# Performance work log

Hardware: AMD Instinct MI355X
Metric: run time of the kernel (lower is better)

## Reference

```python
import jax, jax.numpy as jnp
import numpy as np

N = 100_000      # nodes
E = 3_200_000    # edges (avg degree 32)
F = 16           # irrep feature channels
IR = 4           # (max_l+1)**2 with max_l = 1
DENOM = 32.0     # denominator init kwarg
EPS = 1e-9
INV_S3 = 1.0 / np.sqrt(3.0).astype(np.float32)  # CG norm for 1x1->0
INV_S2 = 1.0 / np.sqrt(2.0).astype(np.float32)  # CG norm for 1x1->1


def setup_inputs() -> dict:
    key = jax.random.key(0)
    k0, k1, k2, k3, k4 = jax.random.split(key, 5)
    positions = jax.random.normal(k0, (N, 3), jnp.float32)
    node_feats = jax.random.normal(k1, (N, F, IR), jnp.float32)
    W = jax.random.normal(k2, (IR, IR), jnp.float32) / np.float32(np.sqrt(IR))
    b = jnp.zeros((IR,), jnp.float32)
    senders = jax.random.randint(k3, (E,), 0, N)
    receivers = jax.random.randint(k4, (E,), 0, N)
    return dict(positions=positions, node_feats=node_feats, W=W, b=b,
                senders=senders, receivers=receivers)


def reference(positions, node_feats, W, b, senders, receivers):
    # --- edge update: SH of normalized relative position, CG tensor product ---
    d = positions[receivers] - positions[senders]               # [E, 3]
    d = d / (jnp.linalg.norm(d, axis=-1, keepdims=True) + EPS)  # unit direction
    # real spherical harmonics up to l=1: sh0 = 1, sh1 = unit direction
    sh1 = d[:, None, :]                                         # [E, 1, 3]

    x = node_feats[senders]                                     # [E, F, 4]
    x0 = x[..., 0:1]                                            # l=0 part [E,F,1]
    x1 = x[..., 1:4]                                            # l=1 part [E,F,3]

    # CG paths with l3 <= max_l = 1:
    #   0x0->0 (identity), 1x1->0 (dot / sqrt3)
    out0 = x0 + jnp.sum(x1 * sh1, axis=-1, keepdims=True) * INV_S3      # [E,F,1]
    #   0x1->1, 1x0->1 (identities), 1x1->1 (cross / sqrt2)
    cross = jnp.cross(x1, jnp.broadcast_to(sh1, x1.shape))
    out1 = x0 * sh1 + x1 + cross * INV_S2                               # [E,F,3]
    tp = jnp.concatenate([out0, out1], axis=-1)                         # [E,F,4]

    # --- node update: segment-sum over receivers, scale, Dense over coeff dim ---
    agg = jax.ops.segment_sum(tp, receivers, num_segments=positions.shape[0])
    agg = agg / DENOM                                                   # [N,F,4]
    return agg @ W + b                                                  # [N,F,4]
```

## Files before the change

### kernel.cpp

```cpp
#include <hip/hip_runtime.h>


#define F_DIM 16
#define BIN_SHIFT 6
#define BIN_NODES (1 << BIN_SHIFT)
#define HALF_NODES (BIN_NODES / 2)
#define CHUNK 8192
#define CAP_LDS 1408
#define MAXBINS 2048

__global__ void __launch_bounds__(256) init_kernel(int* __restrict__ binCur,
                                                   int nbins, int cap)
{
    int b = blockIdx.x * blockDim.x + threadIdx.x;
    if (b < nbins) binCur[b] = b * cap;
}

__global__ void __launch_bounds__(256) pos_pack_kernel(
    const float* __restrict__ pos, float4* __restrict__ posf4, int N)
{
    int n = blockIdx.x * blockDim.x + threadIdx.x;
    if (n >= N) return;
    posf4[n] = make_float4(pos[3*n], pos[3*n+1], pos[3*n+2], 0.f);
}

__global__ void __launch_bounds__(512) build_bins_kernel(
    const int* __restrict__ senders, const int* __restrict__ receivers,
    int* __restrict__ binCur, int* __restrict__ bins,
    int nbins, int cap, int E)
{
    __shared__ int hbase[MAXBINS];
    __shared__ int hrank[MAXBINS];
    int t = threadIdx.x;
    for (int i = t; i < nbins; i += 512) { hbase[i] = 0; hrank[i] = 0; }
    __syncthreads();

    int base = blockIdx.x * CHUNK;
    int end  = base + CHUNK; if (end > E) end = E;

    for (int e = base + t; e < end; e += 512)
        atomicAdd(&hbase[((unsigned)receivers[e]) >> BIN_SHIFT], 1);
    __syncthreads();

    for (int i = t; i < nbins; i += 512) {
        int c = hbase[i];
        hbase[i] = (c > 0) ? atomicAdd(&binCur[i], c) : 0;
    }
    __syncthreads();

    for (int e = base + t; e < end; e += 512) {
        int r = receivers[e];
        int s = senders[e];
        int bb = r >> BIN_SHIFT;
        int rank = atomicAdd(&hrank[bb], 1);
        int dest = hbase[bb] + rank;
        if (dest < (bb + 1) * cap)
            bins[dest] = (s << BIN_SHIFT) | (r & (BIN_NODES - 1));
    }
}

__device__ __forceinline__ void edge_acc_d(
    float dx, float dy, float dz, const float4& fx,
    float& a0, float& a1, float& a2, float& a3)
{
    const float INV_S3 = 0.5773502691896258f;
    const float INV_S2 = 0.7071067811865476f;
    float dot = fx.y*dx + fx.z*dy + fx.w*dz;
    a0 += fx.x + dot * INV_S3;
    float c0 = fx.z*dz - fx.w*dy;
    float c1 = fx.w*dx - fx.y*dz;
    float c2 = fx.y*dy - fx.z*dx;
    a1 += fx.x*dx + fx.y + c0 * INV_S2;
    a2 += fx.x*dy + fx.z + c1 * INV_S2;
    a3 += fx.x*dz + fx.w + c2 * INV_S2;
}

__global__ void __launch_bounds__(256) bin_gather_kernel(
    const float4* __restrict__ posf4,
    const float* __restrict__ nf,
    const int* __restrict__ bins,
    const int* __restrict__ binCur,
    const float* __restrict__ W,
    const float* __restrict__ Bias,
    float* __restrict__ out,
    int N, int cap)
{
    __shared__ float4 ledge[CAP_LDS];
    __shared__ int lhist[HALF_NODES];
    __shared__ int lscan[HALF_NODES];
    __shared__ int lstart[HALF_NODES];

    int t = threadIdx.x;
    int bin  = blockIdx.x >> 1;
    int half = blockIdx.x & 1;
    int node0 = (bin << BIN_SHIFT) + half * HALF_NODES;
    int gbase = bin * cap;

    int cnt = binCur[bin] - gbase;
    if (cnt > cap) cnt = cap;

    if (t < HALF_NODES) lhist[t] = 0;
    __syncthreads();

    for (int j = t; j < cnt; j += 256) {
        int rl = bins[gbase + j] & (BIN_NODES - 1);
        if ((rl >> 5) == half) atomicAdd(&lhist[rl & (HALF_NODES - 1)], 1);
    }
    __syncthreads();

    if (t < HALF_NODES) lscan[t] = lhist[t];
    __syncthreads();
    for (int off = 1; off < HALF_NODES; off <<= 1) {
        int v = (t < HALF_NODES && t >= off) ? lscan[t - off] : 0;
        __syncthreads();
        if (t < HALF_NODES) lscan[t] += v;
        __syncthreads();
    }
    if (t < HALF_NODES) { lstart[t] = lscan[t] - lhist[t]; lhist[t] = 0; }
    __syncthreads();

    for (int j = t; j < cnt; j += 256) {
        int pk = bins[gbase + j];
        int rl = pk & (BIN_NODES - 1);
        if ((rl >> 5) != half) continue;
        int rl32 = rl & (HALF_NODES - 1);
        int s = pk >> BIN_SHIFT;
        int rank = atomicAdd(&lhist[rl32], 1);
        int dest = lstart[rl32] + rank;
        if (dest >= CAP_LDS) continue;
        float4 ps = posf4[s];
        float4 pr = posf4[node0 + rl32];
        float dx = pr.x - ps.x;
        float dy = pr.y - ps.y;
        float dz = pr.z - ps.z;
        float d2 = dx*dx + dy*dy + dz*dz;
        float inv = __builtin_amdgcn_rsqf(fmaxf(d2, 1e-18f));
        float4 rec;
        rec.x = dx * inv;
        rec.y = dy * inv;
        rec.z = dz * inv;
        rec.w = __int_as_float(s);
        ledge[dest] = rec;
    }
    __syncthreads();

    float w[16];
#pragma unroll
    for (int i = 0; i < 16; ++i) w[i] = W[i];
    float b0 = Bias[0], b1 = Bias[1], b2 = Bias[2], b3 = Bias[3];
    const float sc = 1.0f / 32.0f;

    int f = t & 15;
    const float4* nf4 = (const float4*)nf;

    for (int nl = t >> 4; nl < HALF_NODES; nl += 16) {
        int n = node0 + nl;
        if (n >= N) break;
        int s0 = lstart[nl];
        int dcnt = lscan[nl] - s0;
        if (dcnt > CAP_LDS - s0) dcnt = CAP_LDS - s0;

        float a0 = 0.f, a1 = 0.f, a2 = 0.f, a3 = 0.f;
        int j = 0;
        for (; j + 4 <= dcnt; j += 4) {
            float4 e0 = ledge[s0 + j + 0];
            float4 e1 = ledge[s0 + j + 1];
            float4 e2 = ledge[s0 + j + 2];
            float4 e3 = ledge[s0 + j + 3];
            int s_0 = __float_as_int(e0.w);
            int s_1 = __float_as_int(e1.w);
            int s_2 = __float_as_int(e2.w);
            int s_3 = __float_as_int(e3.w);
            float4 q0 = nf4[(unsigned)(s_0 * F_DIM + f)];
            float4 q1 = nf4[(unsigned)(s_1 * F_DIM + f)];
            float4 q2 = nf4[(unsigned)(s_2 * F_DIM + f)];
            float4 q3 = nf4[(unsigned)(s_3 * F_DIM + f)];
            edge_acc_d(e0.x, e0.y, e0.z, q0, a0, a1, a2, a3);
            edge_acc_d(e1.x, e1.y, e1.z, q1, a0, a1, a2, a3);
            edge_acc_d(e2.x, e2.y, e2.z, q2, a0, a1, a2, a3);
            edge_acc_d(e3.x, e3.y, e3.z, q3, a0, a1, a2, a3);
        }
        for (; j < dcnt; ++j) {
            float4 e0 = ledge[s0 + j];
            int s = __float_as_int(e0.w);
            float4 q = nf4[(unsigned)(s * F_DIM + f)];
            edge_acc_d(e0.x, e0.y, e0.z, q, a0, a1, a2, a3);
        }

        a0 *= sc; a1 *= sc; a2 *= sc; a3 *= sc;
        float4 o;
        o.x = a0*w[0] + a1*w[4] + a2*w[8]  + a3*w[12] + b0;
        o.y = a0*w[1] + a1*w[5] + a2*w[9]  + a3*w[13] + b1;
        o.z = a0*w[2] + a1*w[6] + a2*w[10] + a3*w[14] + b2;
        o.w = a0*w[3] + a1*w[7] + a2*w[11] + a3*w[15] + b3;
        ((float4*)out)[(size_t)n * F_DIM + f] = o;
    }
}

__global__ void __launch_bounds__(256) hist_kernel(
    const int* __restrict__ receivers, int* __restrict__ deg,
    int* __restrict__ rank, int E)
{
    int e = blockIdx.x * blockDim.x + threadIdx.x;
    if (e >= E) return;
    rank[e] = atomicAdd(&deg[receivers[e]], 1);
}

__global__ void __launch_bounds__(256) alloc_kernel(
    const int* __restrict__ deg, int* __restrict__ start,
    int* __restrict__ cursor, int N)
{
    __shared__ int tmp[256];
    __shared__ int base;
    int t = threadIdx.x;
    int n = blockIdx.x * blockDim.x + t;
    int v = (n < N) ? deg[n] : 0;
    tmp[t] = v;
    __syncthreads();
    for (int off = 1; off < 256; off <<= 1) {
        int x = (t >= off) ? tmp[t - off] : 0;
        __syncthreads();
        tmp[t] += x;
        __syncthreads();
    }
    int incl = tmp[t];
    if (t == 255) base = atomicAdd(cursor, incl);
    __syncthreads();
    if (n < N) start[n] = base + incl - v;
}

__global__ void __launch_bounds__(256) scatter_kernel(
    const int* __restrict__ senders, const int* __restrict__ receivers,
    const int* __restrict__ rank, const int* __restrict__ start,
    int* __restrict__ csr_s, int E)
{
    int e = blockIdx.x * blockDim.x + threadIdx.x;
    if (e >= E) return;
    csr_s[start[receivers[e]] + rank[e]] = senders[e];
}

__global__ void __launch_bounds__(256) gather_kernel(
    const float* __restrict__ pos,
    const float* __restrict__ nf,
    const int* __restrict__ csr_s,
    const int* __restrict__ start,
    const int* __restrict__ deg,
    const float* __restrict__ W,
    const float* __restrict__ b,
    float* __restrict__ out,
    int N)
{
    const float INV_S3 = 0.5773502691896258f;
    const float INV_S2 = 0.7071067811865476f;

    int tid = blockIdx.x * blockDim.x + threadIdx.x;
    int n = tid >> 4;
    if (n >= N) return;
    int f = tid & 15;

    float rx = pos[3*n], ry = pos[3*n+1], rz = pos[3*n+2];
    int s0 = start[n];
    int dcnt = deg[n];
    float a0 = 0.f, a1 = 0.f, a2 = 0.f, a3 = 0.f;
    const float4* nf4 = (const float4*)nf;

    int s = (dcnt > 0) ? csr_s[s0] : 0;
    for (int j = 0; j < dcnt; ++j) {
        int s_next = (j + 1 < dcnt) ? csr_s[s0 + j + 1] : 0;
        float dx = rx - pos[3*s], dy = ry - pos[3*s+1], dz = rz - pos[3*s+2];
        float d2 = dx*dx + dy*dy + dz*dz;
        float inv = __builtin_amdgcn_rsqf(fmaxf(d2, 1e-18f));
        dx *= inv; dy *= inv; dz *= inv;
        float4 x = nf4[(unsigned)(s * F_DIM + f)];
        float x0 = x.x, x1 = x.y, x2 = x.z, x3 = x.w;
        float dot = x1*dx + x2*dy + x3*dz;
        a0 += x0 + dot * INV_S3;
        float c0 = x2*dz - x3*dy, c1 = x3*dx - x1*dz, c2 = x1*dy - x2*dx;
        a1 += x0*dx + x1 + c0 * INV_S2;
        a2 += x0*dy + x2 + c1 * INV_S2;
        a3 += x0*dz + x3 + c2 * INV_S2;
        s = s_next;
    }
    const float sc = 1.0f / 32.0f;
    a0 *= sc; a1 *= sc; a2 *= sc; a3 *= sc;
    float4 o;
    o.x = a0*W[0] + a1*W[4] + a2*W[8]  + a3*W[12] + b[0];
    o.y = a0*W[1] + a1*W[5] + a2*W[9]  + a3*W[13] + b[1];
    o.z = a0*W[2] + a1*W[6] + a2*W[10] + a3*W[14] + b[2];
    o.w = a0*W[3] + a1*W[7] + a2*W[11] + a3*W[15] + b[3];
    ((float4*)out)[tid] = o;
}

extern "C" void kernel_launch(void* const* d_in, const int* in_sizes, int n_in,
                              void* d_out, int out_size, void* d_ws, size_t ws_size,
                              hipStream_t stream)
{
    const float* pos       = (const float*)d_in[0];
    const float* nf        = (const float*)d_in[1];
    const float* W         = (const float*)d_in[2];
    const float* b         = (const float*)d_in[3];
    const int*   senders   = (const int*)d_in[4];
    const int*   receivers = (const int*)d_in[5];

    int N = in_sizes[0] / 3;
    int E = in_sizes[4];
    float* out = (float*)d_out;
    const int blk = 256;

    int nbins = (N + BIN_NODES - 1) >> BIN_SHIFT;
    int cap   = E / nbins + 453;
    size_t need = ((size_t)N * 4 + (size_t)nbins * cap + nbins) * sizeof(float);

    if (nbins <= MAXBINS && ws_size >= need) {
        float4* posf4 = (float4*)d_ws;
        int* binCur = (int*)(posf4 + N);
        int* bins   = binCur + nbins;

        pos_pack_kernel<<<(N + blk - 1) / blk, blk, 0, stream>>>(pos, posf4, N);
        init_kernel<<<(nbins + blk - 1) / blk, blk, 0, stream>>>(binCur, nbins, cap);
        build_bins_kernel<<<(E + CHUNK - 1) / CHUNK, 512, 0, stream>>>(
            senders, receivers, binCur, bins, nbins, cap, E);
        bin_gather_kernel<<<nbins * 2, blk, 0, stream>>>(
            posf4, nf, bins, binCur, W, b, out, N, cap);
    } else {
        int* cursor = (int*)d_ws;
        int* deg    = cursor + 1;
        int* start  = deg + N;
        int* rank   = start + N;
        int* csr_s  = rank + E;

        hipMemsetAsync(cursor, 0, (size_t)(1 + N) * sizeof(int), stream);
        hist_kernel<<<(E + blk - 1) / blk, blk, 0, stream>>>(receivers, deg, rank, E);
        alloc_kernel<<<(N + blk - 1) / blk, blk, 0, stream>>>(deg, start, cursor, N);
        scatter_kernel<<<(E + blk - 1) / blk, blk, 0, stream>>>(
            senders, receivers, rank, start, csr_s, E);
        long total = (long)N * F_DIM;
        gather_kernel<<<(unsigned)((total + blk - 1) / blk), blk, 0, stream>>>(
            pos, nf, csr_s, start, deg, W, b, out, N);
    }
}
```

Measured before the change: 290.3 us.

## Gather node features as fp16 and fuse pack/init kernels

Adds a pack kernel that converts node features to half precision once per call, and merges it with the position packing and bin-cursor init into a single launch. The gather kernel then reads 8-byte half4 values per edge instead of 16-byte float4, halving random-gather traffic. The cost is an extra full pass over node features each call and reduced input precision, which may exceed tolerance. The fallback gather loop also drops its sender-index prefetch.

```diff
diff --git a/kernel.cpp b/kernel.cpp
--- a/kernel.cpp
+++ b/kernel.cpp
@@ -1,4 +1,5 @@
 #include <hip/hip_runtime.h>
+#include <hip/hip_fp16.h>
 
 
 #define F_DIM 16
@@ -9,19 +10,26 @@
 #define CAP_LDS 1408
 #define MAXBINS 2048
 
-__global__ void __launch_bounds__(256) init_kernel(int* __restrict__ binCur,
-                                                   int nbins, int cap)
-{
-    int b = blockIdx.x * blockDim.x + threadIdx.x;
-    if (b < nbins) binCur[b] = b * cap;
-}
-
-__global__ void __launch_bounds__(256) pos_pack_kernel(
-    const float* __restrict__ pos, float4* __restrict__ posf4, int N)
-{
-    int n = blockIdx.x * blockDim.x + threadIdx.x;
-    if (n >= N) return;
-    posf4[n] = make_float4(pos[3*n], pos[3*n+1], pos[3*n+2], 0.f);
+__global__ void __launch_bounds__(256) pack_kernel(
+    const float* __restrict__ pos, const float* __restrict__ nf,
+    float4* __restrict__ posf4, uint2* __restrict__ nfh,
+    int* __restrict__ binCur, int N, int nbins, int cap)
+{
+    int tid = blockIdx.x * blockDim.x + threadIdx.x;
+    int total = N * F_DIM;
+    if (tid < total) {
+        float4 q = ((const float4*)nf)[tid];
+        __half2 h01 = __floats2half2_rn(q.x, q.y);
+        __half2 h23 = __floats2half2_rn(q.z, q.w);
+        uint2 u;
+        u.x = *reinterpret_cast<unsigned*>(&h01);
+        u.y = *reinterpret_cast<unsigned*>(&h23);
+        nfh[tid] = u;
+    }
+    if (tid < N)
+        posf4[tid] = make_float4(pos[3*tid], pos[3*tid+1], pos[3*tid+2], 0.f);
+    if (tid < nbins)
+        binCur[tid] = tid * cap;
 }
 
 __global__ void __launch_bounds__(512) build_bins_kernel(
@@ -57,6 +65,15 @@
         if (dest < (bb + 1) * cap)
             bins[dest] = (s << BIN_SHIFT) | (r & (BIN_NODES - 1));
     }
+}
+
+__device__ __forceinline__ float4 unpack_h4(uint2 u)
+{
+    __half2 h01 = *reinterpret_cast<__half2*>(&u.x);
+    __half2 h23 = *reinterpret_cast<__half2*>(&u.y);
+    float2 a = __half22float2(h01);
+    float2 b = __half22float2(h23);
+    return make_float4(a.x, a.y, b.x, b.y);
 }
 
 __device__ __forceinline__ void edge_acc_d(
@@ -77,7 +94,7 @@
 
 __global__ void __launch_bounds__(256) bin_gather_kernel(
     const float4* __restrict__ posf4,
-    const float* __restrict__ nf,
+    const uint2* __restrict__ nfh,
     const int* __restrict__ bins,
     const int* __restrict__ binCur,
     const float* __restrict__ W,
@@ -151,7 +168,6 @@
     const float sc = 1.0f / 32.0f;
 
     int f = t & 15;
-    const float4* nf4 = (const float4*)nf;
 
     for (int nl = t >> 4; nl < HALF_NODES; nl += 16) {
         int n = node0 + nl;
@@ -171,20 +187,20 @@
             int s_1 = __float_as_int(e1.w);
             int s_2 = __float_as_int(e2.w);
             int s_3 = __float_as_int(e3.w);
-            float4 q0 = nf4[(unsigned)(s_0 * F_DIM + f)];
-            float4 q1 = nf4[(unsigned)(s_1 * F_DIM + f)];
-            float4 q2 = nf4[(unsigned)(s_2 * F_DIM + f)];
-            float4 q3 = nf4[(unsigned)(s_3 * F_DIM + f)];
-            edge_acc_d(e0.x, e0.y, e0.z, q0, a0, a1, a2, a3);
-            edge_acc_d(e1.x, e1.y, e1.z, q1, a0, a1, a2, a3);
-            edge_acc_d(e2.x, e2.y, e2.z, q2, a0, a1, a2, a3);
-            edge_acc_d(e3.x, e3.y, e3.z, q3, a0, a1, a2, a3);
+            uint2 u0 = nfh[(unsigned)(s_0 * F_DIM + f)];
+            uint2 u1 = nfh[(unsigned)(s_1 * F_DIM + f)];
+            uint2 u2 = nfh[(unsigned)(s_2 * F_DIM + f)];
+            uint2 u3 = nfh[(unsigned)(s_3 * F_DIM + f)];
+            edge_acc_d(e0.x, e0.y, e0.z, unpack_h4(u0), a0, a1, a2, a3);
+            edge_acc_d(e1.x, e1.y, e1.z, unpack_h4(u1), a0, a1, a2, a3);
+            edge_acc_d(e2.x, e2.y, e2.z, unpack_h4(u2), a0, a1, a2, a3);
+            edge_acc_d(e3.x, e3.y, e3.z, unpack_h4(u3), a0, a1, a2, a3);
         }
         for (; j < dcnt; ++j) {
             float4 e0 = ledge[s0 + j];
             int s = __float_as_int(e0.w);
-            float4 q = nf4[(unsigned)(s * F_DIM + f)];
-            edge_acc_d(e0.x, e0.y, e0.z, q, a0, a1, a2, a3);
+            uint2 u = nfh[(unsigned)(s * F_DIM + f)];
+            edge_acc_d(e0.x, e0.y, e0.z, unpack_h4(u), a0, a1, a2, a3);
         }
 
         a0 *= sc; a1 *= sc; a2 *= sc; a3 *= sc;
@@ -264,22 +280,19 @@
     float a0 = 0.f, a1 = 0.f, a2 = 0.f, a3 = 0.f;
     const float4* nf4 = (const float4*)nf;
 
-    int s = (dcnt > 0) ? csr_s[s0] : 0;
     for (int j = 0; j < dcnt; ++j) {
-        int s_next = (j + 1 < dcnt) ? csr_s[s0 + j + 1] : 0;
+        int s = csr_s[s0 + j];
         float dx = rx - pos[3*s], dy = ry - pos[3*s+1], dz = rz - pos[3*s+2];
         float d2 = dx*dx + dy*dy + dz*dz;
         float inv = __builtin_amdgcn_rsqf(fmaxf(d2, 1e-18f));
         dx *= inv; dy *= inv; dz *= inv;
         float4 x = nf4[(unsigned)(s * F_DIM + f)];
-        float x0 = x.x, x1 = x.y, x2 = x.z, x3 = x.w;
-        float dot = x1*dx + x2*dy + x3*dz;
-        a0 += x0 + dot * INV_S3;
-        float c0 = x2*dz - x3*dy, c1 = x3*dx - x1*dz, c2 = x1*dy - x2*dx;
-        a1 += x0*dx + x1 + c0 * INV_S2;
-        a2 += x0*dy + x2 + c1 * INV_S2;
-        a3 += x0*dz + x3 + c2 * INV_S2;
-        s = s_next;
+        float dot = x.y*dx + x.z*dy + x.w*dz;
+        a0 += x.x + dot * INV_S3;
+        float c0 = x.z*dz - x.w*dy, c1 = x.w*dx - x.y*dz, c2 = x.y*dy - x.z*dx;
+        a1 += x.x*dx + x.y + c0 * INV_S2;
+        a2 += x.x*dy + x.z + c1 * INV_S2;
+        a3 += x.x*dz + x.w + c2 * INV_S2;
     }
     const float sc = 1.0f / 32.0f;
     a0 *= sc; a1 *= sc; a2 *= sc; a3 *= sc;
@@ -309,19 +322,22 @@
 
     int nbins = (N + BIN_NODES - 1) >> BIN_SHIFT;
     int cap   = E / nbins + 453;
-    size_t need = ((size_t)N * 4 + (size_t)nbins * cap + nbins) * sizeof(float);
+    size_t need = (size_t)N * 16 + (size_t)N * F_DIM * 8
+                + ((size_t)nbins + (size_t)nbins * cap) * 4;
 
     if (nbins <= MAXBINS && ws_size >= need) {
         float4* posf4 = (float4*)d_ws;
-        int* binCur = (int*)(posf4 + N);
+        uint2*  nfh   = (uint2*)(posf4 + N);
+        int* binCur = (int*)(nfh + (size_t)N * F_DIM);
         int* bins   = binCur + nbins;
 
-        pos_pack_kernel<<<(N + blk - 1) / blk, blk, 0, stream>>>(pos, posf4, N);
-        init_kernel<<<(nbins + blk - 1) / blk, blk, 0, stream>>>(binCur, nbins, cap);
+        int total = N * F_DIM;
+        pack_kernel<<<(total + blk - 1) / blk, blk, 0, stream>>>(
+            pos, nf, posf4, nfh, binCur, N, nbins, cap);
         build_bins_kernel<<<(E + CHUNK - 1) / CHUNK, 512, 0, stream>>>(
             senders, receivers, binCur, bins, nbins, cap, E);
         bin_gather_kernel<<<nbins * 2, blk, 0, stream>>>(
-            posf4, nf, bins, binCur, W, b, out, N, cap);
+            posf4, nfh, bins, binCur, W, b, out, N, cap);
     } else {
         int* cursor = (int*)d_ws;
         int* deg    = cursor + 1;
```

Result: faster. 239.7 us (-17.4%).
